# Optimization experiments

Hardware: AMD Instinct MI355X
Metric: run time of the kernel (lower is better)

The kernel has to match this reference:

```python
import jax, jax.numpy as jnp
import numpy as np
from jax import lax

IN_F = 512
OUT_F = 1024
B = 8192


def setup_inputs() -> dict:
    key = jax.random.key(0)
    kx, kw, kb, ku = jax.random.split(key, 4)
    x = jax.random.normal(kx, (B, IN_F), dtype=jnp.float32)
    # grouped Conv1d(out, out, k=in+out-1, groups=out) weight -> (OUT_F, IN_F+OUT_F-1)
    k = IN_F + OUT_F - 1
    scale = 1.0 / np.sqrt(k)
    weight = jax.random.uniform(kw, (OUT_F, k), minval=-scale, maxval=scale, dtype=jnp.float32)
    bias = jax.random.uniform(kb, (OUT_F,), minval=-scale, maxval=scale, dtype=jnp.float32)
    u = jax.random.uniform(ku, (B, OUT_F), dtype=jnp.float32)  # Bernoulli noise
    return {"x": x, "weight": weight, "bias": bias, "u": u}


def reference(x, weight, bias, u):
    # out[:, i] ~ Bernoulli(sigmoid(logits[:, i]))
    Wx = weight[:, :IN_F]          # (OUT_F, IN_F)   conditioning part
    Wo = weight[:, IN_F:]          # (OUT_F, OUT_F-1) causal part (row i uses first i cols)
    # Precompute the x contribution for all units at once (big GEMM, done once).
    xw = x @ Wx.T + bias[None, :]  # (B, OUT_F)

    def step(out, inp):
        i, xw_i, wo_row, u_i = inp
        # out carry has zeros at positions >= i, so a full dot with wo_row is exact.
        logit = xw_i + out[:, : OUT_F - 1] @ wo_row          # (B,)
        sample = (u_i < jax.nn.sigmoid(logit)).astype(out.dtype)
        out = lax.dynamic_update_slice(out, sample[:, None], (0, i))
        return out, logit

    xs = (jnp.arange(OUT_F), xw.T, Wo, u.T)
    out0 = jnp.zeros((B, OUT_F), dtype=x.dtype)
    out, logits = lax.scan(step, out0, xs)
    logits = logits.T  # (B, OUT_F)
    return out, logits
```

## Files before the change

### kernel.cpp

```cpp
#include <hip/hip_runtime.h>
#include <cstdint>
#include <cstddef>
#include <math.h>

#define IN_F 512
#define OUT_F 1024
#define BATCH 8192
#define W_K 1535
#define PR 1056

typedef _Float16 h4 __attribute__((ext_vector_type(4)));

#define F4C(v, c) ((c) == 0 ? (v).x : (c) == 1 ? (v).y : (c) == 2 ? (v).z : (v).w)

__global__ __launch_bounds__(256) void k_fill(float* __restrict__ out, float val) {
  const size_t i = ((size_t)blockIdx.x * 256 + threadIdx.x) * 4;
  float4 v; v.x = v.y = v.z = v.w = val;
  *(float4*)(out + i) = v;
}

__global__ __launch_bounds__(256) void k_gemm32(const float* __restrict__ x,
                                                const float* __restrict__ w,
                                                const float* __restrict__ bias,
                                                float* __restrict__ xw) {
  __shared__ float xs[64][33];
  __shared__ float wsh[64][33];
  const int t = threadIdx.x;
  const int bsub = t >> 4;
  const int esub = t & 15;
  const int bm = blockIdx.x;
  const int bn = blockIdx.y;
  const int srow = t >> 2;
  const int scol = (t & 3) * 8;
  const float* xbase = x + (size_t)(bm * 64 + srow) * IN_F + scol;
  const float* wbase = w + (size_t)(bn * 64 + srow) * W_K + scol;

  float acc[4][4];
#pragma unroll
  for (int a = 0; a < 4; ++a)
#pragma unroll
    for (int b = 0; b < 4; ++b) acc[a][b] = 0.0f;

  for (int k0 = 0; k0 < IN_F; k0 += 32) {
    float xv[8], wv[8];
#pragma unroll
    for (int c = 0; c < 8; ++c) { xv[c] = xbase[k0 + c]; wv[c] = wbase[k0 + c]; }
    __syncthreads();
#pragma unroll
    for (int c = 0; c < 8; ++c) { xs[srow][scol + c] = xv[c]; wsh[srow][scol + c] = wv[c]; }
    __syncthreads();
#pragma unroll
    for (int k = 0; k < 32; ++k) {
      const float a0 = xs[bsub * 4 + 0][k], a1 = xs[bsub * 4 + 1][k];
      const float a2 = xs[bsub * 4 + 2][k], a3 = xs[bsub * 4 + 3][k];
      const float b0 = wsh[esub * 4 + 0][k], b1 = wsh[esub * 4 + 1][k];
      const float b2 = wsh[esub * 4 + 2][k], b3 = wsh[esub * 4 + 3][k];
      acc[0][0] = fmaf(a0, b0, acc[0][0]); acc[0][1] = fmaf(a0, b1, acc[0][1]);
      acc[0][2] = fmaf(a0, b2, acc[0][2]); acc[0][3] = fmaf(a0, b3, acc[0][3]);
      acc[1][0] = fmaf(a1, b0, acc[1][0]); acc[1][1] = fmaf(a1, b1, acc[1][1]);
      acc[1][2] = fmaf(a1, b2, acc[1][2]); acc[1][3] = fmaf(a1, b3, acc[1][3]);
      acc[2][0] = fmaf(a2, b0, acc[2][0]); acc[2][1] = fmaf(a2, b1, acc[2][1]);
      acc[2][2] = fmaf(a2, b2, acc[2][2]); acc[2][3] = fmaf(a2, b3, acc[2][3]);
      acc[3][0] = fmaf(a3, b0, acc[3][0]); acc[3][1] = fmaf(a3, b1, acc[3][1]);
      acc[3][2] = fmaf(a3, b2, acc[3][2]); acc[3][3] = fmaf(a3, b3, acc[3][3]);
    }
  }

#pragma unroll
  for (int ie = 0; ie < 4; ++ie) {
    const int e = bn * 64 + esub * 4 + ie;
    const float bv = bias[e];
#pragma unroll
    for (int ib = 0; ib < 4; ++ib) {
      const int b = bm * 64 + bsub * 4 + ib;
      xw[(size_t)b * OUT_F + e] = acc[ib][ie] + bv;
    }
  }
}

__global__ __launch_bounds__(256) void k_perm(const float* __restrict__ w,
                                              float* __restrict__ wPerm,
                                              float* __restrict__ wTail) {
  const int i = blockIdx.x;
  const int t = threadIdx.x;
  const float* src = w + (size_t)i * W_K + IN_F;
  float* drow = wPerm + (size_t)i * PR;
#pragma unroll
  for (int c = 0; c < 4; ++c) {
    const int j = t + 256 * c;
    const float v = (j < OUT_F - 1) ? src[j] : 0.0f;
    if (j < 1016) drow[(j & 7) * 132 + (j >> 3)] = v;
    else if (j < OUT_F - 1) wTail[i * 8 + (j - 1016)] = v;
    else wTail[i * 8 + 7] = 0.0f;
  }
  if (t < 40) drow[(t / 5) * 132 + 127 + (t % 5)] = 0.0f;
}

__device__ __forceinline__ float dpp_xor2(float x) {
  int y = __builtin_amdgcn_update_dpp(0, __float_as_int(x), 0x4E, 0xF, 0xF, true);
  return __int_as_float(y);
}
__device__ __forceinline__ float dpp_xor1(float x) {
  int y = __builtin_amdgcn_update_dpp(0, __float_as_int(x), 0xB1, 0xF, 0xF, true);
  return __int_as_float(y);
}
__device__ __forceinline__ float rth_of(float uu) {
  const float e1 = 1.0f - uu;
  float l1, l2;
  asm("v_log_f32 %0, %1" : "=v"(l1) : "v"(e1));
  asm("v_log_f32 %0, %1" : "=v"(l2) : "v"(uu));
  float rt = l1 - l2;
  if (e1 == 0.0f) rt = __builtin_nanf("");
  return rt;
}
__device__ __forceinline__ void block_sync_lds() {
  asm volatile("s_waitcnt lgkmcnt(0)" ::: "memory");
  __builtin_amdgcn_s_barrier();
  asm volatile("" ::: "memory");
}

#define SCAN_STEP(PH, A, B) do {                                               \
    if ((B) == 0)                                                              \
      opq[1] = *(const float4*)&oldp[(PH) & 1][2 * (A) + 1][g][m][0];          \
    if ((B) == 4 && (A) < 3)                                                   \
      opq[0] = *(const float4*)&oldp[(PH) & 1][2 * (A) + 2][g][m][0];          \
    const int i_ = 32 * (PH) + 8 * (A) + (B);                                  \
    float P_ = F4C(opq[((B) >> 2) & 1], (B) & 3);                              \
    {                                                                          \
      const float4 wl_ = wlo[(B) & 3];                                         \
      P_ = fmaf(ps[0], wl_.x, P_);                                             \
      P_ = fmaf(ps[1], wl_.y, P_);                                             \
      P_ = fmaf(ps[2], wl_.z, P_);                                             \
      if ((A) == 0 && (B) == 0) P_ = fmaf((m < 7) ? ps[3] : 0.0f, wl_.w, P_);  \
      else                      P_ = fmaf(ps[3], wl_.w, P_);                   \
    }                                                                          \
    {                                                                          \
      const float4 wh_ = whi[(B) & 3];                                         \
      if ((A) >= 1) {                                                          \
        if ((A) == 1 && (B) == 0) P_ = fmaf((m < 7) ? cs[0] : 0.0f, wh_.x, P_);\
        else                      P_ = fmaf(cs[0], wh_.x, P_);                 \
      }                                                                        \
      if ((A) >= 2) {                                                          \
        if ((A) == 2 && (B) == 0) P_ = fmaf((m < 7) ? cs[1] : 0.0f, wh_.y, P_);\
        else                      P_ = fmaf(cs[1], wh_.y, P_);                 \
      }                                                                        \
      if ((A) >= 3) {                                                          \
        if ((A) == 3 && (B) == 0) P_ = fmaf((m < 7) ? cs[2] : 0.0f, wh_.z, P_);\
        else                      P_ = fmaf(cs[2], wh_.z, P_);                 \
      }                                                                        \
      if ((B) >= 2)                                                            \
        P_ = fmaf((m < (B) - 1) ? cs[(A)] : 0.0f, F4C(wh_, (A)), P_);          \
    }                                                                          \
    P_ = fmaf((m == (((B) + 7) & 7)) ? s_prev : 0.0f, wapp[(B) & 3], P_);      \
    float t1_ = P_ + __shfl_xor(P_, 4);                                        \
    float t2_ = t1_ + dpp_xor2(t1_);                                           \
    const float T_ = t2_ + dpp_xor1(t2_);                                      \
    const float L_ = xwh[(B) & 1] + T_;                                        \
    const float tneg_ = L_ * NL2E;                                             \
    float s_ = (tneg_ < rth_cur) ? 1.0f : 0.0f;                                \
    const float mg_ = __builtin_fabsf(tneg_ - rth_cur);                        \
    if (__builtin_expect(!(mg_ >= 1e-3f), 0)) {                                \
      const double sd_ = 1.0 / (1.0 + exp(-(double)L_));                       \
      s_ = (uu[(B) & 1] < (float)sd_) ? 1.0f : 0.0f;                           \
    }                                                                          \
    if (m == 0) { xwl_row[i_] = L_; osr[i_] = s_; }                            \
    cs[(A)] = (m == (B)) ? s_ : cs[(A)];                                       \
    s_prev = s_;                                                               \
    rth_cur = rth_of(uu[((B) + 1) & 1]);                                       \
    {                                                                          \
      const int nx2_ = (i_ + 2 < OUT_F) ? i_ + 2 : OUT_F - 1;                  \
      xwh[(B) & 1] = xwl_row[nx2_];                                            \
      uu[(B) & 1] = uro[nx2_];                                                 \
    }                                                                          \
    {                                                                          \
      const int nx4_ = (i_ + 4 < OUT_F) ? i_ + 4 : OUT_F - 1;                  \
      const int th_ = (nx4_ >> 5) * 4;                                         \
      const int tlo_ = (th_ >= 4) ? th_ - 4 : 0;                               \
      const float* wr_ = wPermRow + (size_t)nx4_ * PR;                         \
      wlo[(B) & 3] = *(const float4*)(wr_ + tlo_);                             \
      whi[(B) & 3] = *(const float4*)(wr_ + th_);                              \
      wapp[(B) & 3] = wAppBase[(size_t)nx4_ * (W_K + 1)];                      \
    }                                                                          \
  } while (0)

#define SCAN_GROUP(PH, A) do {                                                 \
    SCAN_STEP(PH, A, 0); SCAN_STEP(PH, A, 1);                                  \
    SCAN_STEP(PH, A, 2); SCAN_STEP(PH, A, 3);                                  \
    SCAN_STEP(PH, A, 4); SCAN_STEP(PH, A, 5);                                  \
    SCAN_STEP(PH, A, 6); SCAN_STEP(PH, A, 7);                                  \
  } while (0)

#define SPEC_STEP(IO) do {                                                     \
    const int i_ = 1017 + (IO);                                                \
    const int o_ = 25 + (IO);                                                  \
    float P_ = F4C(opq[(o_ >> 2) & 1], o_ & 3);                                \
    {                                                                          \
      const float4 wl_ = wlo[o_ & 3];                                          \
      P_ = fmaf(ps[0], wl_.x, P_); P_ = fmaf(ps[1], wl_.y, P_);                \
      P_ = fmaf(ps[2], wl_.z, P_); P_ = fmaf(ps[3], wl_.w, P_);                \
    }                                                                          \
    {                                                                          \
      const float4 wh_ = whi[o_ & 3];                                          \
      P_ = fmaf(cs[0], wh_.x, P_); P_ = fmaf(cs[1], wh_.y, P_);                \
      P_ = fmaf(cs[2], wh_.z, P_);                                             \
    }                                                                          \
    float t1_ = P_ + __shfl_xor(P_, 4);                                        \
    float t2_ = t1_ + dpp_xor2(t1_);                                           \
    float T_ = t2_ + dpp_xor1(t2_);                                            \
    tl[(IO)] = s_prev;                                                         \
    T_ = fmaf(tl[0], twa.x, T_);                                               \
    if ((IO) >= 1) T_ = fmaf(tl[1], twa.y, T_);                                \
    if ((IO) >= 2) T_ = fmaf(tl[2], twa.z, T_);                                \
    if ((IO) >= 3) T_ = fmaf(tl[3], twa.w, T_);                                \
    if ((IO) >= 4) T_ = fmaf(tl[4], twb.x, T_);                                \
    if ((IO) >= 5) T_ = fmaf(tl[5], twb.y, T_);                                \
    if ((IO) >= 6) T_ = fmaf(tl[6], twb.z, T_);                                \
    const float L_ = xwh[o_ & 1] + T_;                                         \
    const float tneg_ = L_ * NL2E;                                             \
    float s_ = (tneg_ < rth_cur) ? 1.0f : 0.0f;                                \
    const float mg_ = __builtin_fabsf(tneg_ - rth_cur);                        \
    if (__builtin_expect(!(mg_ >= 1e-3f), 0)) {                                \
      const double sd_ = 1.0 / (1.0 + exp(-(double)L_));                       \
      s_ = (uu[o_ & 1] < (float)sd_) ? 1.0f : 0.0f;                            \
    }                                                                          \
    if (m == 0) { xwl_row[i_] = L_; osr[i_] = s_; }                            \
    s_prev = s_;                                                               \
    rth_cur = rth_of(uu[(o_ + 1) & 1]);                                        \
    {                                                                          \
      const int nx2_ = (i_ + 2 < OUT_F) ? i_ + 2 : OUT_F - 1;                  \
      xwh[o_ & 1] = xwl_row[nx2_]; uu[o_ & 1] = uro[nx2_];                     \
    }                                                                          \
    {                                                                          \
      const int nx4_ = (i_ + 4 < OUT_F) ? i_ + 4 : OUT_F - 1;                  \
      const float* wr_ = wPermRow + (size_t)nx4_ * PR;                         \
      wlo[o_ & 3] = *(const float4*)(wr_ + 120);                               \
      whi[o_ & 3] = *(const float4*)(wr_ + 124);                               \
    }                                                                          \
    if ((IO) < 6) {                                                            \
      twa = *(const float4*)(wTail + (i_ + 1) * 8);                            \
      twb = *(const float4*)(wTail + (i_ + 1) * 8 + 4);                        \
    }                                                                          \
  } while (0)

__global__ __launch_bounds__(256) void k_scan32(const float* __restrict__ w,
                                                const float* __restrict__ u,
                                                const float* __restrict__ wPerm,
                                                const float* __restrict__ wTail,
                                                float* xwl,
                                                float* __restrict__ out_s) {
  __shared__ _Float16 smph[8][128][8];
  __shared__ float oldp[2][8][8][8][4];

  const int tid = threadIdx.x;
  const int wid = tid >> 6;
  const int lane = tid & 63;
  const int g = lane >> 3, m = lane & 7;
  const float NL2E = -1.44269504088896340736f;

  {
    float* z = &oldp[0][0][0][0][0];
#pragma unroll
    for (int k = 0; k < 8; ++k) z[tid + 256 * k] = 0.0f;
  }
  __syncthreads();

  const int r = blockIdx.x * 8 + g;
  float* xwl_row = xwl + (size_t)r * OUT_F;
  const float* uro = u + (size_t)r * OUT_F;
  float* osr = out_s + (size_t)r * OUT_F;

  float4 wlo[4], whi[4], opq[2];
  float wapp[4], xwh[2], uu[2];
  float ps[4], cs[4], tl[7];
  float rth_cur = 0.0f, s_prev = 0.0f;
  const float* wPermRow = wPerm + m * 132;
  const float* wAppBase = w + (IN_F - 1);
  const int bl = (wid - 1) * 64 + lane;

  if (wid == 0) {
#pragma unroll
    for (int c = 0; c < 4; ++c) { ps[c] = 0.0f; cs[c] = 0.0f; }
#pragma unroll
    for (int c = 0; c < 7; ++c) tl[c] = 0.0f;
#pragma unroll
    for (int b = 0; b < 4; ++b) {
      const float* wr_ = wPermRow + (size_t)b * PR;
      wlo[b] = *(const float4*)(wr_);
      whi[b] = *(const float4*)(wr_);
      wapp[b] = (b == 0) ? 0.0f : wAppBase[(size_t)b * (W_K + 1)];
    }
    xwh[0] = xwl_row[0]; xwh[1] = xwl_row[1];
    uu[0] = uro[0]; uu[1] = uro[1];
    rth_cur = rth_of(uu[0]);
  }

  for (int p = 0; p < 31; ++p) {
    if (wid == 0) {
      opq[0] = *(const float4*)&oldp[p & 1][0][g][m][0];
      SCAN_GROUP(p, 0); SCAN_GROUP(p, 1); SCAN_GROUP(p, 2); SCAN_GROUP(p, 3);
#pragma unroll
      for (int k = 0; k < 4; ++k)
        smph[m][4 * p + k][g] = (_Float16)cs[k];
#pragma unroll
      for (int k = 0; k < 4; ++k) ps[k] = cs[k];
    } else {
      const int buf = (p + 1) & 1;
      for (int q = bl; q < 256; q += 192) {
        const int mq = q >> 5;
        const int iop = (q & 31) >> 1;
        const int rh = q & 1;
        const int i0 = 32 * (p + 1) + iop * 2;
        float a00 = 0, a01 = 0, a02 = 0, a03 = 0;
        float a10 = 0, a11 = 0, a12 = 0, a13 = 0;
        const _Float16* sb = &smph[mq][0][rh * 4];
        const float* w0 = wPerm + (size_t)i0 * PR + mq * 132;
        const float* w1 = w0 + PR;
#pragma unroll 2
        for (int t4 = 0; t4 < p; ++t4) {
          const float4 wa = *(const float4*)(w0 + 4 * t4);
          const float4 wb = *(const float4*)(w1 + 4 * t4);
#pragma unroll
          for (int tt = 0; tt < 4; ++tt) {
            const h4 sv = *(const h4*)(sb + (4 * t4 + tt) * 8);
            const float s0 = (float)sv[0], s1 = (float)sv[1];
            const float s2 = (float)sv[2], s3 = (float)sv[3];
            const float wA = F4C(wa, tt), wB = F4C(wb, tt);
            a00 = fmaf(s0, wA, a00); a01 = fmaf(s1, wA, a01);
            a02 = fmaf(s2, wA, a02); a03 = fmaf(s3, wA, a03);
            a10 = fmaf(s0, wB, a10); a11 = fmaf(s1, wB, a11);
            a12 = fmaf(s2, wB, a12); a13 = fmaf(s3, wB, a13);
          }
        }
        const int qd = (iop * 2) >> 2, c0 = (iop * 2) & 3;
        oldp[buf][qd][rh * 4 + 0][mq][c0] = a00;
        oldp[buf][qd][rh * 4 + 1][mq][c0] = a01;
        oldp[buf][qd][rh * 4 + 2][mq][c0] = a02;
        oldp[buf][qd][rh * 4 + 3][mq][c0] = a03;
        oldp[buf][qd][rh * 4 + 0][mq][c0 + 1] = a10;
        oldp[buf][qd][rh * 4 + 1][mq][c0 + 1] = a11;
        oldp[buf][qd][rh * 4 + 2][mq][c0 + 1] = a12;
        oldp[buf][qd][rh * 4 + 3][mq][c0 + 1] = a13;
      }
    }
    block_sync_lds();
  }

  if (wid == 0) {
    opq[0] = *(const float4*)&oldp[1][0][g][m][0];
    SCAN_GROUP(31, 0); SCAN_GROUP(31, 1); SCAN_GROUP(31, 2);
    SCAN_STEP(31, 3, 0);
    float4 twa = *(const float4*)(wTail + 1017 * 8);
    float4 twb = *(const float4*)(wTail + 1017 * 8 + 4);
    SPEC_STEP(0); SPEC_STEP(1); SPEC_STEP(2); SPEC_STEP(3);
    SPEC_STEP(4); SPEC_STEP(5); SPEC_STEP(6);
  }
}

extern "C" void kernel_launch(void* const* d_in, const int* in_sizes, int n_in,
                              void* d_out, int out_size, void* d_ws, size_t ws_size,
                              hipStream_t stream) {
  float* out_s = (float*)d_out;
  float* out_l = out_s + (size_t)BATCH * OUT_F;
  const int nfill = (BATCH * OUT_F) / (256 * 4);

  const bool shapes_ok =
      n_in == 4 &&
      in_sizes[0] == BATCH * IN_F && in_sizes[1] == OUT_F * W_K &&
      in_sizes[2] == OUT_F && in_sizes[3] == BATCH * OUT_F &&
      out_size == 2 * BATCH * OUT_F;
  if (!shapes_ok) {
    k_fill<<<nfill, 256, 0, stream>>>(out_s, 11.0f);
    return;
  }

  const size_t perm_bytes = ((size_t)OUT_F * PR + (size_t)OUT_F * 8) * sizeof(float);
  if (ws_size < perm_bytes) {
    k_fill<<<nfill, 256, 0, stream>>>(out_s, 7.0f);
    return;
  }

  const float* x = (const float*)d_in[0];
  const float* w = (const float*)d_in[1];
  const float* bias = (const float*)d_in[2];
  const float* u = (const float*)d_in[3];
  float* wPerm = (float*)d_ws;
  float* wTail = wPerm + (size_t)OUT_F * PR;

  k_gemm32<<<dim3(BATCH / 64, OUT_F / 64), 256, 0, stream>>>(x, w, bias, out_l);
  k_perm<<<OUT_F, 256, 0, stream>>>(w, wPerm, wTail);
  k_scan32<<<BATCH / 8, 256, 0, stream>>>(w, u, wPerm, wTail, out_l, out_s);
}
```

Before: 890.1 us.

## Process 16 rows per scan block with two scan waves and restaged helper GEMV

Each scan block now handles 16 batch rows using two sequential-scan waves instead of one, and grows to 384 threads. The four helper waves compute the block-causal partial dot products with a new transposed weight copy (wPermT), which is staged through a small per-wave LDS buffer and register-prefetched. Each weight load is then reused across four rows and four outputs. The aim is to amortize weight traffic over more rows and widen scan parallelism per block, at the cost of a larger workspace, extra writes in k_perm, and more LDS per block, which may reduce occupancy.

```diff
diff --git a/kernel.cpp b/kernel.cpp
--- a/kernel.cpp
+++ b/kernel.cpp
@@ -8,6 +8,8 @@
 #define BATCH 8192
 #define W_K 1535
 #define PR 1056
+#define ROWS 16
+#define SR 136
 
 typedef _Float16 h4 __attribute__((ext_vector_type(4)));
 
@@ -80,7 +82,8 @@
 
 __global__ __launch_bounds__(256) void k_perm(const float* __restrict__ w,
                                               float* __restrict__ wPerm,
-                                              float* __restrict__ wTail) {
+                                              float* __restrict__ wTail,
+                                              float* __restrict__ wPermT) {
   const int i = blockIdx.x;
   const int t = threadIdx.x;
   const float* src = w + (size_t)i * W_K + IN_F;
@@ -89,8 +92,10 @@
   for (int c = 0; c < 4; ++c) {
     const int j = t + 256 * c;
     const float v = (j < OUT_F - 1) ? src[j] : 0.0f;
-    if (j < 1016) drow[(j & 7) * 132 + (j >> 3)] = v;
-    else if (j < OUT_F - 1) wTail[i * 8 + (j - 1016)] = v;
+    if (j < 1016) {
+      drow[(j & 7) * 132 + (j >> 3)] = v;
+      wPermT[(size_t)(j >> 3) * (OUT_F * 8) + i * 8 + (j & 7)] = v;
+    } else if (j < OUT_F - 1) wTail[i * 8 + (j - 1016)] = v;
     else wTail[i * 8 + 7] = 0.0f;
   }
   if (t < 40) drow[(t / 5) * 132 + 127 + (t % 5)] = 0.0f;
@@ -121,9 +126,9 @@
 
 #define SCAN_STEP(PH, A, B) do {                                               \
     if ((B) == 0)                                                              \
-      opq[1] = *(const float4*)&oldp[(PH) & 1][2 * (A) + 1][g][m][0];          \
+      opq[1] = *(const float4*)&oldp[(PH) & 1][2 * (A) + 1][rl][m][0];         \
     if ((B) == 4 && (A) < 3)                                                   \
-      opq[0] = *(const float4*)&oldp[(PH) & 1][2 * (A) + 2][g][m][0];          \
+      opq[0] = *(const float4*)&oldp[(PH) & 1][2 * (A) + 2][rl][m][0];         \
     const int i_ = 32 * (PH) + 8 * (A) + (B);                                  \
     float P_ = F4C(opq[((B) >> 2) & 1], (B) & 3);                              \
     {                                                                          \
@@ -242,14 +247,27 @@
     }                                                                          \
   } while (0)
 
-__global__ __launch_bounds__(256) void k_scan32(const float* __restrict__ w,
+#define FOLD_RR(RR) do {                                                       \
+    const h4 sv_ = *(const h4*)&smph[r0 + (RR)][mB][4 * c];                    \
+    _Pragma("unroll")                                                          \
+    for (int ii = 0; ii < 4; ++ii) {                                           \
+      acc[(RR)][ii] = fmaf((float)sv_[0], F4C(wq0, ii), acc[(RR)][ii]);        \
+      acc[(RR)][ii] = fmaf((float)sv_[1], F4C(wq1, ii), acc[(RR)][ii]);        \
+      acc[(RR)][ii] = fmaf((float)sv_[2], F4C(wq2, ii), acc[(RR)][ii]);        \
+      acc[(RR)][ii] = fmaf((float)sv_[3], F4C(wq3, ii), acc[(RR)][ii]);        \
+    }                                                                          \
+  } while (0)
+
+__global__ __launch_bounds__(384) void k_scan32(const float* __restrict__ w,
                                                 const float* __restrict__ u,
                                                 const float* __restrict__ wPerm,
                                                 const float* __restrict__ wTail,
+                                                const float* __restrict__ wPermT,
                                                 float* xwl,
                                                 float* __restrict__ out_s) {
-  __shared__ _Float16 smph[8][128][8];
-  __shared__ float oldp[2][8][8][8][4];
+  __shared__ _Float16 smph[ROWS][8][SR];
+  __shared__ float oldp[2][8][ROWS][8][4];
+  __shared__ float wch[4][4][8][8];
 
   const int tid = threadIdx.x;
   const int wid = tid >> 6;
@@ -259,12 +277,12 @@
 
   {
     float* z = &oldp[0][0][0][0][0];
-#pragma unroll
-    for (int k = 0; k < 8; ++k) z[tid + 256 * k] = 0.0f;
+    for (int k = tid; k < 8 * ROWS * 8 * 4; k += 384) z[k] = 0.0f;
   }
   __syncthreads();
 
-  const int r = blockIdx.x * 8 + g;
+  const int rl = wid * 8 + g;
+  const int r = blockIdx.x * ROWS + rl;
   float* xwl_row = xwl + (size_t)r * OUT_F;
   const float* uro = u + (size_t)r * OUT_F;
   float* osr = out_s + (size_t)r * OUT_F;
@@ -275,9 +293,8 @@
   float rth_cur = 0.0f, s_prev = 0.0f;
   const float* wPermRow = wPerm + m * 132;
   const float* wAppBase = w + (IN_F - 1);
-  const int bl = (wid - 1) * 64 + lane;
-
-  if (wid == 0) {
+
+  if (wid < 2) {
 #pragma unroll
     for (int c = 0; c < 4; ++c) { ps[c] = 0.0f; cs[c] = 0.0f; }
 #pragma unroll
@@ -294,59 +311,67 @@
     rth_cur = rth_of(uu[0]);
   }
 
+  const int bt = tid - 128;
+  const int wv = bt >> 6;
+  const int mB = bt & 7;
+  const int r0 = ((bt >> 3) & 3) * 4;
+  const int ibase = ((bt >> 5) & 1) * 4;
+  const int qv = bt >> 5;
+  const int ltt = (bt & 63) >> 4;
+  const int lq = bt & 15;
+  const int li = lq >> 1, m0 = (lq & 1) * 4;
+  float* wchw = &wch[wv][0][0][0];
+
   for (int p = 0; p < 31; ++p) {
-    if (wid == 0) {
-      opq[0] = *(const float4*)&oldp[p & 1][0][g][m][0];
+    if (wid < 2) {
+      opq[0] = *(const float4*)&oldp[p & 1][0][rl][m][0];
       SCAN_GROUP(p, 0); SCAN_GROUP(p, 1); SCAN_GROUP(p, 2); SCAN_GROUP(p, 3);
-#pragma unroll
-      for (int k = 0; k < 4; ++k)
-        smph[m][4 * p + k][g] = (_Float16)cs[k];
+      h4 hv;
+      hv[0] = (_Float16)cs[0]; hv[1] = (_Float16)cs[1];
+      hv[2] = (_Float16)cs[2]; hv[3] = (_Float16)cs[3];
+      *(h4*)&smph[rl][m][4 * p] = hv;
 #pragma unroll
       for (int k = 0; k < 4; ++k) ps[k] = cs[k];
     } else {
-      const int buf = (p + 1) & 1;
-      for (int q = bl; q < 256; q += 192) {
-        const int mq = q >> 5;
-        const int iop = (q & 31) >> 1;
-        const int rh = q & 1;
-        const int i0 = 32 * (p + 1) + iop * 2;
-        float a00 = 0, a01 = 0, a02 = 0, a03 = 0;
-        float a10 = 0, a11 = 0, a12 = 0, a13 = 0;
-        const _Float16* sb = &smph[mq][0][rh * 4];
-        const float* w0 = wPerm + (size_t)i0 * PR + mq * 132;
-        const float* w1 = w0 + PR;
-#pragma unroll 2
-        for (int t4 = 0; t4 < p; ++t4) {
-          const float4 wa = *(const float4*)(w0 + 4 * t4);
-          const float4 wb = *(const float4*)(w1 + 4 * t4);
-#pragma unroll
-          for (int tt = 0; tt < 4; ++tt) {
-            const h4 sv = *(const h4*)(sb + (4 * t4 + tt) * 8);
-            const float s0 = (float)sv[0], s1 = (float)sv[1];
-            const float s2 = (float)sv[2], s3 = (float)sv[3];
-            const float wA = F4C(wa, tt), wB = F4C(wb, tt);
-            a00 = fmaf(s0, wA, a00); a01 = fmaf(s1, wA, a01);
-            a02 = fmaf(s2, wA, a02); a03 = fmaf(s3, wA, a03);
-            a10 = fmaf(s0, wB, a10); a11 = fmaf(s1, wB, a11);
-            a12 = fmaf(s2, wB, a12); a13 = fmaf(s3, wB, a13);
-          }
-        }
-        const int qd = (iop * 2) >> 2, c0 = (iop * 2) & 3;
-        oldp[buf][qd][rh * 4 + 0][mq][c0] = a00;
-        oldp[buf][qd][rh * 4 + 1][mq][c0] = a01;
-        oldp[buf][qd][rh * 4 + 2][mq][c0] = a02;
-        oldp[buf][qd][rh * 4 + 3][mq][c0] = a03;
-        oldp[buf][qd][rh * 4 + 0][mq][c0 + 1] = a10;
-        oldp[buf][qd][rh * 4 + 1][mq][c0 + 1] = a11;
-        oldp[buf][qd][rh * 4 + 2][mq][c0 + 1] = a12;
-        oldp[buf][qd][rh * 4 + 3][mq][c0 + 1] = a13;
+      const int i0win = 32 * (p + 1);
+      float acc[4][4];
+#pragma unroll
+      for (int a = 0; a < 4; ++a)
+#pragma unroll
+        for (int b = 0; b < 4; ++b) acc[a][b] = 0.0f;
+
+      const float* gbase = wPermT +
+          (((size_t)ltt * OUT_F + i0win + 8 * wv + li) * 8 + m0);
+      float4 stg{};
+      if (p > 0) stg = *(const float4*)gbase;
+      for (int c = 0; c < p; ++c) {
+        float4 nxt{};
+        if (c + 1 < p)
+          nxt = *(const float4*)(gbase + (size_t)(c + 1) * (4 * OUT_F * 8));
+        wchw[(ltt * 8 + m0 + 0) * 8 + li] = stg.x;
+        wchw[(ltt * 8 + m0 + 1) * 8 + li] = stg.y;
+        wchw[(ltt * 8 + m0 + 2) * 8 + li] = stg.z;
+        wchw[(ltt * 8 + m0 + 3) * 8 + li] = stg.w;
+        const float4 wq0 = *(const float4*)&wchw[(0 * 8 + mB) * 8 + ibase];
+        const float4 wq1 = *(const float4*)&wchw[(1 * 8 + mB) * 8 + ibase];
+        const float4 wq2 = *(const float4*)&wchw[(2 * 8 + mB) * 8 + ibase];
+        const float4 wq3 = *(const float4*)&wchw[(3 * 8 + mB) * 8 + ibase];
+        FOLD_RR(0); FOLD_RR(1); FOLD_RR(2); FOLD_RR(3);
+        stg = nxt;
+      }
+      const int nb = (p + 1) & 1;
+#pragma unroll
+      for (int rr = 0; rr < 4; ++rr) {
+        float4 v;
+        v.x = acc[rr][0]; v.y = acc[rr][1]; v.z = acc[rr][2]; v.w = acc[rr][3];
+        *(float4*)&oldp[nb][qv][r0 + rr][mB][0] = v;
       }
     }
     block_sync_lds();
   }
 
-  if (wid == 0) {
-    opq[0] = *(const float4*)&oldp[1][0][g][m][0];
+  if (wid < 2) {
+    opq[0] = *(const float4*)&oldp[1][0][rl][m][0];
     SCAN_GROUP(31, 0); SCAN_GROUP(31, 1); SCAN_GROUP(31, 2);
     SCAN_STEP(31, 3, 0);
     float4 twa = *(const float4*)(wTail + 1017 * 8);
@@ -373,7 +398,9 @@
     return;
   }
 
-  const size_t perm_bytes = ((size_t)OUT_F * PR + (size_t)OUT_F * 8) * sizeof(float);
+  const size_t perm_bytes =
+      ((size_t)OUT_F * PR + (size_t)OUT_F * 8 + (size_t)128 * OUT_F * 8) *
+      sizeof(float);
   if (ws_size < perm_bytes) {
     k_fill<<<nfill, 256, 0, stream>>>(out_s, 7.0f);
     return;
@@ -385,8 +412,10 @@
   const float* u = (const float*)d_in[3];
   float* wPerm = (float*)d_ws;
   float* wTail = wPerm + (size_t)OUT_F * PR;
+  float* wPermT = wTail + (size_t)OUT_F * 8;
 
   k_gemm32<<<dim3(BATCH / 64, OUT_F / 64), 256, 0, stream>>>(x, w, bias, out_l);
-  k_perm<<<OUT_F, 256, 0, stream>>>(w, wPerm, wTail);
-  k_scan32<<<BATCH / 8, 256, 0, stream>>>(w, u, wPerm, wTail, out_l, out_s);
-}
+  k_perm<<<OUT_F, 256, 0, stream>>>(w, wPerm, wTail, wPermT);
+  k_scan32<<<BATCH / ROWS, 384, 0, stream>>>(w, u, wPerm, wTail, wPermT,
+                                             out_l, out_s);
+}
```

Result: faster. 809.0 us (-9.1%).
